# Kernel optimization log

Hardware: AMD Instinct MI355X
Metric: run time of the kernel (lower is better)

Reference implementation:

```python
import jax, jax.numpy as jnp
import numpy as np

N_NODES = 100000
N_EDGES = 1600000
D_IN = 128
D_OUT = 128


def setup_inputs() -> dict:
    key = jax.random.key(0)
    k_h, k_w, k_s, k_d = jax.random.split(key, 4)
    h = jax.random.normal(k_h, (N_NODES, D_IN), dtype=jnp.float32)
    W = jax.random.normal(k_w, (D_IN, D_OUT), dtype=jnp.float32) * (1.0 / np.sqrt(D_IN))
    b = jnp.zeros((D_OUT,), dtype=jnp.float32)
    src = jax.random.randint(k_s, (N_EDGES,), 0, N_NODES, dtype=jnp.int32)
    dst = jax.random.randint(k_d, (N_EDGES,), 0, N_NODES, dtype=jnp.int32)
    # add self loops (as in the docstring example) so every node has degree >= 1
    loops = jnp.arange(N_NODES, dtype=jnp.int32)
    src = jnp.concatenate([src, loops])
    dst = jnp.concatenate([dst, loops])
    return {"h": h, "W": W, "b": b, "src": src, "dst": dst}


def reference(h, W, b, src, dst):
    N = h.shape[0]
    # update_all(copy_u, sum): gather source features, scatter-sum to destinations
    agg = jax.ops.segment_sum(h[src], dst, num_segments=N)  # [N, d_in]
    # out_degrees: count of outgoing edges per node
    deg = jax.ops.segment_sum(jnp.ones_like(src, dtype=h.dtype), src, num_segments=N)  # [N]
    norm = (deg ** -0.5)[:, None]  # [N, 1]
    # h = activation(kernel(norm * h) * norm + bias); activation is identity, dropout=0
    out = ((norm * agg) @ W) * norm + b
    return out
```

## Files before the change

kernel.cpp:

```cpp
#include <hip/hip_runtime.h>

#define D 128
#define CHUNK 8192
#define NCHUNK_MAX 256
#define BSH 7
#define BUCKET 128
#define NB_MAX 1024
#define STAGE_CAP 3072

__device__ __forceinline__ unsigned int pack_bf16(float a, float b) {
    unsigned int ua = __float_as_uint(a), ub = __float_as_uint(b);
    ua = (ua + 0x7fffu + ((ua >> 16) & 1u)) >> 16;
    ub = (ub + 0x7fffu + ((ub >> 16) & 1u)) >> 16;
    return (ub << 16) | (ua & 0xffffu);
}

struct Phase1Smem {
    union {
        struct {
            int hist[NB_MAX];
            unsigned int stage[CHUNK];
        } p;
        struct {
            float tile[64][D];
        } g;
    };
};

__global__ __launch_bounds__(256) void phase1(const float* __restrict__ h,
                                              const float* __restrict__ Wm,
                                              const int* __restrict__ src,
                                              const int* __restrict__ dst,
                                              unsigned int* __restrict__ pairs,
                                              int* __restrict__ cnt_g,
                                              int* __restrict__ loff_g,
                                              int* __restrict__ outdeg,
                                              unsigned int* __restrict__ hw,
                                              int E, int nb, int nchunk, int N) {
    __shared__ Phase1Smem sm;
    const int t = threadIdx.x;

    if ((int)blockIdx.x < nchunk) {
        __builtin_amdgcn_s_setprio(1);
        const int c  = blockIdx.x;
        const int e0 = c * CHUNK;
        const int n  = min(CHUNK, E - e0);

        for (int i = t; i < nb; i += 256) sm.p.hist[i] = 0;
        __syncthreads();

        for (int i = t; i < n; i += 256) {
            int d = dst[e0 + i];
            atomicAdd(&sm.p.hist[d >> BSH], 1);
        }
        __syncthreads();

        for (int i = t; i < nb; i += 256) cnt_g[(size_t)c * nb + i] = sm.p.hist[i];
        __syncthreads();

        if (t == 0) {
            int acc = 0;
            for (int i = 0; i < nb; ++i) { int v = sm.p.hist[i]; sm.p.hist[i] = acc; acc += v; }
        }
        __syncthreads();

        for (int i = t; i < nb; i += 256) loff_g[(size_t)c * nb + i] = sm.p.hist[i];
        __syncthreads();

        for (int i = t; i < n; i += 256) {
            int d = dst[e0 + i];
            int s = src[e0 + i];
            atomicAdd(&outdeg[s], 1);
            int slot = atomicAdd(&sm.p.hist[d >> BSH], 1);
            sm.p.stage[slot] = ((unsigned int)(d & (BUCKET - 1)) << 24) | (unsigned int)s;
        }
        __syncthreads();

        for (int i = t; i < n; i += 256) pairs[e0 + i] = sm.p.stage[i];
        __builtin_amdgcn_s_setprio(0);
    } else {
        const int r0 = ((int)blockIdx.x - nchunk) * 64;

        #pragma unroll
        for (int i = 0; i < 8; ++i) {
            int flat4 = i * 256 + t;
            int r     = flat4 >> 5;
            int c4    = flat4 & 31;
            int gr    = r0 + r;
            float4 v  = make_float4(0.f, 0.f, 0.f, 0.f);
            if (gr < N) v = reinterpret_cast<const float4*>(h + (size_t)gr * D)[c4];
            reinterpret_cast<float4*>(&sm.g.tile[r][c4 * 4])[0] = v;
        }
        __syncthreads();

        const int wsel = t >> 6;
        const int cp   = t & 63;
        const int j0   = cp * 2;

        float acc[16][2];
        #pragma unroll
        for (int r = 0; r < 16; ++r) { acc[r][0] = 0.f; acc[r][1] = 0.f; }

        for (int k = 0; k < D; k += 4) {
            float2 w[4];
            #pragma unroll
            for (int kk = 0; kk < 4; ++kk)
                w[kk] = reinterpret_cast<const float2*>(Wm + (size_t)(k + kk) * D + j0)[0];
            #pragma unroll
            for (int r = 0; r < 16; ++r) {
                float4 a = reinterpret_cast<const float4*>(&sm.g.tile[wsel * 16 + r][k])[0];
                acc[r][0] += a.x * w[0].x + a.y * w[1].x + a.z * w[2].x + a.w * w[3].x;
                acc[r][1] += a.x * w[0].y + a.y * w[1].y + a.z * w[2].y + a.w * w[3].y;
            }
        }

        #pragma unroll
        for (int r = 0; r < 16; ++r) {
            int gr = r0 + wsel * 16 + r;
            if (gr < N) hw[(size_t)gr * 64 + cp] = pack_bf16(acc[r][0], acc[r][1]);
        }
    }
}

__global__ __launch_bounds__(512) void sort_agg(const unsigned int* __restrict__ pairs,
                                                const int* __restrict__ cnt_g,
                                                const int* __restrict__ loff_g,
                                                const unsigned int* __restrict__ hw,
                                                const int* __restrict__ outdeg,
                                                const float* __restrict__ bias,
                                                float* __restrict__ out,
                                                int nb, int nchunk, int N) {
    __shared__ int sec_base[NCHUNK_MAX + 1];
    __shared__ int sec_lo[NCHUNK_MAX];
    __shared__ int dstart[BUCKET + 1];
    __shared__ int dcur[BUCKET];
    __shared__ unsigned int stage[STAGE_CAP];

    const int t = threadIdx.x;
    const int b = blockIdx.x;

    for (int c = t; c < nchunk; c += 512) {
        sec_base[c] = cnt_g[(size_t)c * nb + b];
        sec_lo[c]   = loff_g[(size_t)c * nb + b];
    }
    if (t < BUCKET) dstart[t] = 0;
    __syncthreads();
    if (t == 0) {
        int acc = 0;
        for (int c = 0; c < nchunk; ++c) { int v = sec_base[c]; sec_base[c] = acc; acc += v; }
        sec_base[nchunk] = acc;
    }
    __syncthreads();

    const int total = sec_base[nchunk];

    for (int j = t; j < total; j += 512) {
        int lo = 0, hi = nchunk - 1;
        while (lo < hi) { int mid = (lo + hi + 1) >> 1; if (sec_base[mid] <= j) lo = mid; else hi = mid - 1; }
        unsigned int p = pairs[(size_t)lo * CHUNK + sec_lo[lo] + (j - sec_base[lo])];
        atomicAdd(&dstart[p >> 24], 1);
    }
    __syncthreads();

    if (t == 0) {
        int acc = 0;
        for (int i = 0; i < BUCKET; ++i) { int v = dstart[i]; dstart[i] = acc; acc += v; }
        dstart[BUCKET] = acc;
    }
    __syncthreads();
    if (t < BUCKET) dcur[t] = dstart[t];
    __syncthreads();

    const int wav  = t >> 6;
    const int lane = t & 63;
    const float2 bb = reinterpret_cast<const float2*>(bias)[lane];

    if (total <= STAGE_CAP) {
        for (int j = t; j < total; j += 512) {
            int lo = 0, hi = nchunk - 1;
            while (lo < hi) { int mid = (lo + hi + 1) >> 1; if (sec_base[mid] <= j) lo = mid; else hi = mid - 1; }
            unsigned int p = pairs[(size_t)lo * CHUNK + sec_lo[lo] + (j - sec_base[lo])];
            int slot = atomicAdd(&dcur[p >> 24], 1);
            stage[slot] = p & 0xFFFFFFu;
        }
        __syncthreads();

        for (int r = wav; r < BUCKET; r += 8) {
            const int node = (b << BSH) + r;
            if (node >= N) break;
            const int e0 = dstart[r], e1 = dstart[r + 1];
            float ax = 0.f, ay = 0.f;
            int e = e0;
            for (; e + 8 <= e1; e += 8) {
                int sx[8];
                #pragma unroll
                for (int q = 0; q < 8; ++q) sx[q] = (int)stage[e + q];
                unsigned int u[8];
                #pragma unroll
                for (int q = 0; q < 8; ++q) u[q] = hw[(size_t)sx[q] * 64 + lane];
                #pragma unroll
                for (int q = 0; q < 8; ++q) {
                    ax += __uint_as_float(u[q] << 16);
                    ay += __uint_as_float(u[q] & 0xffff0000u);
                }
            }
            for (; e + 4 <= e1; e += 4) {
                int s0 = (int)stage[e],     s1 = (int)stage[e + 1];
                int s2 = (int)stage[e + 2], s3 = (int)stage[e + 3];
                unsigned int u0 = hw[(size_t)s0 * 64 + lane];
                unsigned int u1 = hw[(size_t)s1 * 64 + lane];
                unsigned int u2 = hw[(size_t)s2 * 64 + lane];
                unsigned int u3 = hw[(size_t)s3 * 64 + lane];
                ax += __uint_as_float(u0 << 16) + __uint_as_float(u1 << 16)
                    + __uint_as_float(u2 << 16) + __uint_as_float(u3 << 16);
                ay += __uint_as_float(u0 & 0xffff0000u) + __uint_as_float(u1 & 0xffff0000u)
                    + __uint_as_float(u2 & 0xffff0000u) + __uint_as_float(u3 & 0xffff0000u);
            }
            for (; e < e1; ++e) {
                unsigned int u = hw[(size_t)stage[e] * 64 + lane];
                ax += __uint_as_float(u << 16);
                ay += __uint_as_float(u & 0xffff0000u);
            }
            float sc = 1.0f / (float)outdeg[node];
            float2 o;
            o.x = ax * sc + bb.x;
            o.y = ay * sc + bb.y;
            reinterpret_cast<float2*>(out + (size_t)node * D)[lane] = o;
        }
    } else {
        for (int r = wav; r < BUCKET; r += 8) {
            const int node = (b << BSH) + r;
            if (node >= N) break;
            float ax = 0.f, ay = 0.f;
            for (int c = 0; c < nchunk; ++c) {
                const int cb = sec_base[c], ce = sec_base[c + 1];
                const size_t pb = (size_t)c * CHUNK + sec_lo[c];
                for (int j = cb; j < ce; ++j) {
                    unsigned int p = pairs[pb + (j - cb)];
                    if ((int)(p >> 24) == r) {
                        unsigned int u = hw[(size_t)(p & 0xFFFFFFu) * 64 + lane];
                        ax += __uint_as_float(u << 16);
                        ay += __uint_as_float(u & 0xffff0000u);
                    }
                }
            }
            float sc = 1.0f / (float)outdeg[node];
            float2 o;
            o.x = ax * sc + bb.x;
            o.y = ay * sc + bb.y;
            reinterpret_cast<float2*>(out + (size_t)node * D)[lane] = o;
        }
    }
}

__global__ void deg_kernel(const int* __restrict__ src, int* __restrict__ deg, int E) {
    int i = blockIdx.x * blockDim.x + threadIdx.x;
    int stride = gridDim.x * blockDim.x;
    for (; i < E; i += stride) atomicAdd(&deg[src[i]], 1);
}

__global__ void scatter_kernel(const float* __restrict__ h,
                               const int* __restrict__ src,
                               const int* __restrict__ dst,
                               float* __restrict__ agg, int E) {
    int wave   = (int)((blockIdx.x * blockDim.x + threadIdx.x) >> 6);
    int lane   = threadIdx.x & 63;
    int nwaves = (int)((gridDim.x * blockDim.x) >> 6);
    for (int e = wave; e < E; e += nwaves) {
        int s = src[e];
        int d = dst[e];
        const float2 v = reinterpret_cast<const float2*>(h + (size_t)s * D)[lane];
        float* arow = agg + (size_t)d * D + lane * 2;
        atomicAdd(arow + 0, v.x);
        atomicAdd(arow + 1, v.y);
    }
}

__global__ __launch_bounds__(256) void gemm_finish(float* __restrict__ out,
                                                   const float* __restrict__ Wm,
                                                   const float* __restrict__ bias,
                                                   const int* __restrict__ deg,
                                                   int N) {
    __shared__ __align__(16) float tile[64][D];
    const int r0 = blockIdx.x * 64;
    const int t  = threadIdx.x;

    #pragma unroll
    for (int i = 0; i < 8; ++i) {
        int flat4 = i * 256 + t;
        int r     = flat4 >> 5;
        int c4    = flat4 & 31;
        int gr    = r0 + r;
        float4 v  = make_float4(0.f, 0.f, 0.f, 0.f);
        if (gr < N) v = reinterpret_cast<const float4*>(out + (size_t)gr * D)[c4];
        reinterpret_cast<float4*>(&tile[r][c4 * 4])[0] = v;
    }
    __syncthreads();

    const int wsel = t >> 6;
    const int j0   = (t & 63) * 2;

    float acc[16][2];
    #pragma unroll
    for (int r = 0; r < 16; ++r) { acc[r][0] = 0.f; acc[r][1] = 0.f; }

    for (int k = 0; k < D; k += 4) {
        float2 w[4];
        #pragma unroll
        for (int kk = 0; kk < 4; ++kk)
            w[kk] = reinterpret_cast<const float2*>(Wm + (size_t)(k + kk) * D + j0)[0];
        #pragma unroll
        for (int r = 0; r < 16; ++r) {
            float4 a = reinterpret_cast<const float4*>(&tile[wsel * 16 + r][k])[0];
            acc[r][0] += a.x * w[0].x + a.y * w[1].x + a.z * w[2].x + a.w * w[3].x;
            acc[r][1] += a.x * w[0].y + a.y * w[1].y + a.z * w[2].y + a.w * w[3].y;
        }
    }

    const float2 bb = reinterpret_cast<const float2*>(bias + j0)[0];
    #pragma unroll
    for (int r = 0; r < 16; ++r) {
        int gr = r0 + wsel * 16 + r;
        if (gr < N) {
            float sc = 1.0f / (float)deg[gr];
            float2 o;
            o.x = acc[r][0] * sc + bb.x;
            o.y = acc[r][1] * sc + bb.y;
            reinterpret_cast<float2*>(out + (size_t)gr * D + j0)[0] = o;
        }
    }
}

extern "C" void kernel_launch(void* const* d_in, const int* in_sizes, int n_in,
                              void* d_out, int out_size, void* d_ws, size_t ws_size,
                              hipStream_t stream) {
    const float* h   = (const float*)d_in[0];
    const float* Wm  = (const float*)d_in[1];
    const float* bia = (const float*)d_in[2];
    const int*   src = (const int*)d_in[3];
    const int*   dst = (const int*)d_in[4];
    float*       out = (float*)d_out;

    const int N = in_sizes[0] / D;
    const int E = in_sizes[3];

    const int nb      = (N + BUCKET - 1) >> BSH;
    const int nchunk  = (E + CHUNK - 1) / CHUNK;
    const int gblocks = (N + 63) / 64;

    size_t tier1_ints = (size_t)N + (size_t)2 * nchunk * nb
                      + (size_t)nchunk * CHUNK + (size_t)N * 64;

    bool shape_ok = (N < (1 << 24)) && nb <= NB_MAX && nchunk <= NCHUNK_MAX;

    if (shape_ok && ws_size >= tier1_ints * sizeof(int)) {
        int* outdeg = (int*)d_ws;
        int* cnt_g  = outdeg + N;
        int* loff_g = cnt_g + (size_t)nchunk * nb;
        unsigned int* pairs = (unsigned int*)(loff_g + (size_t)nchunk * nb);
        unsigned int* hw = pairs + (size_t)nchunk * CHUNK;

        hipMemsetAsync(outdeg, 0, (size_t)N * sizeof(int), stream);

        phase1<<<nchunk + gblocks, 256, 0, stream>>>(h, Wm, src, dst, pairs,
                                                     cnt_g, loff_g, outdeg,
                                                     hw, E, nb, nchunk, N);

        sort_agg<<<nb, 512, 0, stream>>>(pairs, cnt_g, loff_g, hw,
                                         outdeg, bia, out, nb, nchunk, N);
    } else {
        int* deg = (int*)d_ws;
        hipMemsetAsync(out, 0, (size_t)out_size * sizeof(float), stream);
        hipMemsetAsync(deg, 0, (size_t)N * sizeof(int), stream);
        deg_kernel<<<2048, 256, 0, stream>>>(src, deg, E);
        scatter_kernel<<<8192, 256, 0, stream>>>(h, src, dst, out, E);
        gemm_finish<<<(N + 63) / 64, 256, 0, stream>>>(out, Wm, bia, deg, N);
    }
}
```

Measured before the change: 199.7 us.

## Compute h@W projection with bf16 MFMA instead of scalar FMA

Replaces the scalar FP32 shared-memory GEMM in phase1's projection blocks with bf16 MFMA 16x16x32 instructions. h is loaded straight from global memory and packed to bf16 in registers, with no shared-memory tile. A small kernel first converts W into a transposed bf16 copy in the workspace. This targets the FMA-bound GEMM part of phase1 and drops the smem union, at the cost of an extra launch and lower input precision for the GEMM.

```diff
diff --git a/kernel.cpp b/kernel.cpp
--- a/kernel.cpp
+++ b/kernel.cpp
@@ -8,6 +8,9 @@
 #define NB_MAX 1024
 #define STAGE_CAP 3072
 
+typedef __attribute__((ext_vector_type(8))) short bf16x8;
+typedef __attribute__((ext_vector_type(4))) float f32x4;
+
 __device__ __forceinline__ unsigned int pack_bf16(float a, float b) {
     unsigned int ua = __float_as_uint(a), ub = __float_as_uint(b);
     ua = (ua + 0x7fffu + ((ua >> 16) & 1u)) >> 16;
@@ -15,20 +18,24 @@
     return (ub << 16) | (ua & 0xffffu);
 }
 
+__global__ __launch_bounds__(256) void conv_w(const float* __restrict__ W,
+                                              unsigned short* __restrict__ Wtb) {
+    int i = blockIdx.x * 256 + threadIdx.x;
+    int col = i >> 7, k = i & 127;
+    unsigned int u = __float_as_uint(W[k * D + col]);
+    u = (u + 0x7fffu + ((u >> 16) & 1u)) >> 16;
+    Wtb[i] = (unsigned short)u;
+}
+
 struct Phase1Smem {
-    union {
-        struct {
-            int hist[NB_MAX];
-            unsigned int stage[CHUNK];
-        } p;
-        struct {
-            float tile[64][D];
-        } g;
-    };
+    struct {
+        int hist[NB_MAX];
+        unsigned int stage[CHUNK];
+    } p;
 };
 
 __global__ __launch_bounds__(256) void phase1(const float* __restrict__ h,
-                                              const float* __restrict__ Wm,
+                                              const unsigned short* __restrict__ Wtb,
                                               const int* __restrict__ src,
                                               const int* __restrict__ dst,
                                               unsigned int* __restrict__ pairs,
@@ -80,44 +87,42 @@
         __builtin_amdgcn_s_setprio(0);
     } else {
         const int r0 = ((int)blockIdx.x - nchunk) * 64;
-
+        const int w  = t >> 6;
+        const int l  = t & 63;
+        const int hr = l & 15;
+        const int cg = l >> 4;
+
+        const int gr  = r0 + w * 16 + hr;
+        const int grc = (gr < N) ? gr : (N - 1);
+
+        f32x4 acc[8];
         #pragma unroll
-        for (int i = 0; i < 8; ++i) {
-            int flat4 = i * 256 + t;
-            int r     = flat4 >> 5;
-            int c4    = flat4 & 31;
-            int gr    = r0 + r;
-            float4 v  = make_float4(0.f, 0.f, 0.f, 0.f);
-            if (gr < N) v = reinterpret_cast<const float4*>(h + (size_t)gr * D)[c4];
-            reinterpret_cast<float4*>(&sm.g.tile[r][c4 * 4])[0] = v;
-        }
-        __syncthreads();
-
-        const int wsel = t >> 6;
-        const int cp   = t & 63;
-        const int j0   = cp * 2;
-
-        float acc[16][2];
+        for (int ct = 0; ct < 8; ++ct) acc[ct] = (f32x4){0.f, 0.f, 0.f, 0.f};
+
         #pragma unroll
-        for (int r = 0; r < 16; ++r) { acc[r][0] = 0.f; acc[r][1] = 0.f; }
-
-        for (int k = 0; k < D; k += 4) {
-            float2 w[4];
+        for (int kg = 0; kg < 4; ++kg) {
+            const float* hp = h + (size_t)grc * D + kg * 32 + cg * 8;
+            float4 h0 = reinterpret_cast<const float4*>(hp)[0];
+            float4 h1 = reinterpret_cast<const float4*>(hp)[1];
+            unsigned int hu[4] = { pack_bf16(h0.x, h0.y), pack_bf16(h0.z, h0.w),
+                                   pack_bf16(h1.x, h1.y), pack_bf16(h1.z, h1.w) };
+            bf16x8 hf = *reinterpret_cast<bf16x8*>(hu);
+
             #pragma unroll
-            for (int kk = 0; kk < 4; ++kk)
-                w[kk] = reinterpret_cast<const float2*>(Wm + (size_t)(k + kk) * D + j0)[0];
+            for (int ct = 0; ct < 8; ++ct) {
+                bf16x8 wf = *reinterpret_cast<const bf16x8*>(
+                    Wtb + ((size_t)(ct * 16 + hr) * D + kg * 32 + cg * 8));
+                acc[ct] = __builtin_amdgcn_mfma_f32_16x16x32_bf16(wf, hf, acc[ct], 0, 0, 0);
+            }
+        }
+
+        if (gr < N) {
             #pragma unroll
-            for (int r = 0; r < 16; ++r) {
-                float4 a = reinterpret_cast<const float4*>(&sm.g.tile[wsel * 16 + r][k])[0];
-                acc[r][0] += a.x * w[0].x + a.y * w[1].x + a.z * w[2].x + a.w * w[3].x;
-                acc[r][1] += a.x * w[0].y + a.y * w[1].y + a.z * w[2].y + a.w * w[3].y;
-            }
-        }
-
-        #pragma unroll
-        for (int r = 0; r < 16; ++r) {
-            int gr = r0 + wsel * 16 + r;
-            if (gr < N) hw[(size_t)gr * 64 + cp] = pack_bf16(acc[r][0], acc[r][1]);
+            for (int ct = 0; ct < 8; ++ct) {
+                int cpb = ct * 8 + cg * 2;
+                hw[(size_t)gr * 64 + cpb]     = pack_bf16(acc[ct][0], acc[ct][1]);
+                hw[(size_t)gr * 64 + cpb + 1] = pack_bf16(acc[ct][2], acc[ct][3]);
+            }
         }
     }
 }
@@ -348,21 +353,24 @@
     const int nchunk  = (E + CHUNK - 1) / CHUNK;
     const int gblocks = (N + 63) / 64;
 
-    size_t tier1_ints = (size_t)N + (size_t)2 * nchunk * nb
+    size_t tier1_ints = (size_t)N + 8192 + (size_t)2 * nchunk * nb
                       + (size_t)nchunk * CHUNK + (size_t)N * 64;
 
     bool shape_ok = (N < (1 << 24)) && nb <= NB_MAX && nchunk <= NCHUNK_MAX;
 
     if (shape_ok && ws_size >= tier1_ints * sizeof(int)) {
         int* outdeg = (int*)d_ws;
-        int* cnt_g  = outdeg + N;
+        unsigned short* Wtb = (unsigned short*)(outdeg + N);
+        int* cnt_g  = (int*)Wtb + 8192;
         int* loff_g = cnt_g + (size_t)nchunk * nb;
         unsigned int* pairs = (unsigned int*)(loff_g + (size_t)nchunk * nb);
         unsigned int* hw = pairs + (size_t)nchunk * CHUNK;
 
         hipMemsetAsync(outdeg, 0, (size_t)N * sizeof(int), stream);
 
-        phase1<<<nchunk + gblocks, 256, 0, stream>>>(h, Wm, src, dst, pairs,
+        conv_w<<<64, 256, 0, stream>>>(Wm, Wtb);
+
+        phase1<<<nchunk + gblocks, 256, 0, stream>>>(h, Wtb, src, dst, pairs,
                                                      cnt_g, loff_g, outdeg,
                                                      hw, E, nb, nchunk, N);
 
```

Result: no change. 199.8 us (+0.1%).
